# Performance work log

Measured on AMD Instinct MI355X. Metric: run time of the kernel, lower is better.

## Reference

```python
import jax, jax.numpy as jnp
import numpy as np

N0, N1, N2, N3 = 100000, 25000, 6250, 1600
DEG = 16
D_IN, D_H = 512, 256


def setup_inputs() -> dict:
    key = jax.random.key(0)
    ks = jax.random.split(key, 20)
    inp = {}
    inp["x"] = jax.random.normal(ks[0], (N0, D_IN), dtype=jnp.float32)
    # bipartite blocks: (src_ids into previous frontier, dst_ids into next frontier)
    inp["src0"] = jax.random.randint(ks[1], (N1 * DEG,), 0, N0)
    inp["dst0"] = jax.random.randint(ks[2], (N1 * DEG,), 0, N1)
    inp["src1"] = jax.random.randint(ks[3], (N2 * DEG,), 0, N1)
    inp["dst1"] = jax.random.randint(ks[4], (N2 * DEG,), 0, N2)
    inp["src2"] = jax.random.randint(ks[5], (N3 * DEG,), 0, N2)
    inp["dst2"] = jax.random.randint(ks[6], (N3 * DEG,), 0, N3)
    def xavier(k, shp):
        fan_in, fan_out = shp
        lim = jnp.sqrt(6.0 / (fan_in + fan_out))
        return jax.random.uniform(k, shp, jnp.float32, -lim, lim)
    inp["Ws0"] = xavier(ks[7], (D_IN, D_H)); inp["Wn0"] = xavier(ks[8], (D_IN, D_H)); inp["b0"] = jnp.zeros((D_H,), jnp.float32)
    inp["Ws1"] = xavier(ks[9], (D_H, D_H)); inp["Wn1"] = xavier(ks[10], (D_H, D_H)); inp["b1"] = jnp.zeros((D_H,), jnp.float32)
    inp["Ws2"] = xavier(ks[11], (D_H, D_H)); inp["Wn2"] = xavier(ks[12], (D_H, D_H)); inp["b2"] = jnp.zeros((D_H,), jnp.float32)
    inp["W_fc"] = xavier(ks[13], (D_H, D_H)); inp["b_fc"] = jnp.zeros((D_H,), jnp.float32)
    return inp


def _sage_mean(h, src, dst, n_dst, Ws, Wn, b):
    # DGL SAGEConv('mean') on a bipartite block: out = h_dst@Ws + mean_neigh@Wn + b
    h_dst = h[:n_dst]                                   # [n_dst, d]
    msg = h[src]                                        # [E, d] gather
    agg = jax.ops.segment_sum(msg, dst, num_segments=n_dst)
    deg = jax.ops.segment_sum(jnp.ones(src.shape, h.dtype), dst, num_segments=n_dst)
    mean = agg / jnp.maximum(deg, 1.0)[:, None]
    return h_dst @ Ws + mean @ Wn + b


def reference(x, src0, dst0, src1, dst1, src2, dst2,
              Ws0, Wn0, b0, Ws1, Wn1, b1, Ws2, Wn2, b2, W_fc, b_fc):
    h = _sage_mean(x, src0, dst0, N1, Ws0, Wn0, b0)
    h = jax.nn.relu(h)  # dropout is identity in eval mode
    h = _sage_mean(h, src1, dst1, N2, Ws1, Wn1, b1)
    h = jax.nn.relu(h)
    h = _sage_mean(h, src2, dst2, N3, Ws2, Wn2, b2)
    return h @ W_fc + b_fc
```

## Files before the change

### kernel.cpp

```cpp
#include <hip/hip_runtime.h>
#include <hip/hip_bf16.h>
#include <cstddef>
#include <cstdint>

#define N0 100000
#define N1 25000
#define N2 6250
#define N3 1600
#define DEG 16
#define D_IN 512
#define D_H 256

#define E0 (N1*DEG)
#define E1 (N2*DEG)
#define E2 (N3*DEG)

typedef _Float16 half_t;
typedef __attribute__((ext_vector_type(8))) _Float16 f16x8;
typedef __attribute__((ext_vector_type(4))) float f32x4;

#define XB 25000
#define WB 2304
#define HB (((E0+E1+E2) + 255) / 256)

__device__ __forceinline__ void gl_lds16(const void* g, void* l)
{
    __builtin_amdgcn_global_load_lds(
        (const __attribute__((address_space(1))) void*)g,
        (__attribute__((address_space(3))) void*)l,
        16, 0, 0);
}

__global__ __launch_bounds__(256)
void mega_conv_kernel(const float* __restrict__ x, half_t* __restrict__ xh,
                      const float* s0, const float* s1, const float* s2, const float* s3,
                      const float* s4, const float* s5, const float* s6,
                      half_t* t0, half_t* t1, half_t* t2, half_t* t3,
                      half_t* t4, half_t* t5, half_t* t6,
                      const int* __restrict__ d0, const int* __restrict__ d1,
                      const int* __restrict__ d2,
                      int* __restrict__ c0, int* __restrict__ c1, int* __restrict__ c2)
{
    const int bid = blockIdx.x;
    if (bid < XB) {
        const int id = bid * 256 + threadIdx.x;
        const float4* p = reinterpret_cast<const float4*>(x) + (size_t)id * 2;
        const float4 a = p[0], b = p[1];
        f16x8 o;
        o[0] = (half_t)a.x; o[1] = (half_t)a.y; o[2] = (half_t)a.z; o[3] = (half_t)a.w;
        o[4] = (half_t)b.x; o[5] = (half_t)b.y; o[6] = (half_t)b.z; o[7] = (half_t)b.w;
        *(reinterpret_cast<f16x8*>(xh) + id) = o;
    } else if (bid < XB + WB) {
        const int id = (bid - XB) * 256 + threadIdx.x;
        const float* src; half_t* dst; int kb; int e;
        if (id < 131072)      { src = s0; dst = t0; kb = 9; e = id; }
        else if (id < 262144) { src = s1; dst = t1; kb = 9; e = id - 131072; }
        else if (id < 327680) { src = s2; dst = t2; kb = 8; e = id - 262144; }
        else if (id < 393216) { src = s3; dst = t3; kb = 8; e = id - 327680; }
        else if (id < 458752) { src = s4; dst = t4; kb = 8; e = id - 393216; }
        else if (id < 524288) { src = s5; dst = t5; kb = 8; e = id - 458752; }
        else if (id < 589824) { src = s6; dst = t6; kb = 8; e = id - 524288; }
        else return;
        const int K = 1 << kb;
        const int nn = e >> kb, k = e & (K - 1);
        dst[((size_t)nn << kb) + k] = (half_t)src[(size_t)k * 256 + nn];
    } else {
        const int i = (bid - XB - WB) * 256 + threadIdx.x;
        if (i < E0)                atomicAdd(&c0[d0[i]], 1);
        else if (i < E0 + E1)      atomicAdd(&c1[d1[i - E0]], 1);
        else if (i < E0 + E1 + E2) atomicAdd(&c2[d2[i - E0 - E1]], 1);
    }
}

__global__ void fill3_kernel(const int* __restrict__ s0, const int* __restrict__ d0,
                             const int* __restrict__ s1, const int* __restrict__ d1,
                             const int* __restrict__ s2, const int* __restrict__ d2,
                             int* __restrict__ u0, int* __restrict__ u1, int* __restrict__ u2,
                             int* __restrict__ e0, int* __restrict__ e1, int* __restrict__ e2)
{
    const int i = blockIdx.x * 256 + threadIdx.x;
    if (i < E0) {
        const int p = atomicAdd(&u0[d0[i]], 1); e0[p] = s0[i];
    } else if (i < E0 + E1) {
        const int j = i - E0;
        const int p = atomicAdd(&u1[d1[j]], 1); e1[p] = s1[j];
    } else if (i < E0 + E1 + E2) {
        const int j = i - E0 - E1;
        const int p = atomicAdd(&u2[d2[j]], 1); e2[p] = s2[j];
    }
}

__global__ __launch_bounds__(1024)
void scan3_kernel(const int* __restrict__ c0, int* __restrict__ p0, int* __restrict__ u0,
                  const int* __restrict__ c1, int* __restrict__ p1, int* __restrict__ u1,
                  const int* __restrict__ c2, int* __restrict__ p2, int* __restrict__ u2)
{
    const int b = blockIdx.x;
    const int* cnt = (b == 0) ? c0 : (b == 1) ? c1 : c2;
    int* ptr = (b == 0) ? p0 : (b == 1) ? p1 : p2;
    int* cur = (b == 0) ? u0 : (b == 1) ? u1 : u2;
    const int n = (b == 0) ? N1 : (b == 1) ? N2 : N3;

    const int t = threadIdx.x;
    const int chunk = (n + 1023) >> 10;
    const int beg = t * chunk;
    const int end = min(n, beg + chunk);

    int sum = 0;
    for (int i = beg; i < end; ++i) sum += cnt[i];

    const int lane = t & 63, wid = t >> 6;
    int inc = sum;
    #pragma unroll
    for (int d = 1; d < 64; d <<= 1) {
        int u = __shfl_up(inc, d, 64);
        if (lane >= d) inc += u;
    }
    __shared__ int wtot[16];
    __shared__ int total_s;
    if (lane == 63) wtot[wid] = inc;
    __syncthreads();
    if (wid == 0) {
        int w = (lane < 16) ? wtot[lane] : 0;
        int ws = w;
        #pragma unroll
        for (int d = 1; d < 16; d <<= 1) {
            int u = __shfl_up(ws, d, 64);
            if (lane >= d) ws += u;
        }
        if (lane < 16) wtot[lane] = ws - w;
        if (lane == 15) total_s = ws;
    }
    __syncthreads();
    int run = (inc - sum) + wtot[wid];
    for (int i = beg; i < end; ++i) {
        ptr[i] = run; cur[i] = run;
        run += cnt[i];
    }
    if (t == 0) ptr[n] = total_s;
}

template<int K>
__global__ __launch_bounds__(256)
void csr_mean_f16(const half_t* __restrict__ h, const int* __restrict__ esrc,
                  const int* __restrict__ ptr, half_t* __restrict__ mean, int n)
{
    constexpr int TPN = K / 8;
    constexpr int NPB = 256 / TPN;
    const int node = blockIdx.x * NPB + threadIdx.x / TPN;
    const int lane = threadIdx.x % TPN;
    if (node >= n) return;
    const int beg = ptr[node], end = ptr[node + 1];
    float acc[8] = {};
    for (int base = beg; base < end; base += TPN) {
        const int rem = end - base;
        const int cnt = (rem < TPN) ? rem : TPN;
        const int myidx = (lane < cnt) ? esrc[base + lane] : 0;
        int j = 0;
        for (; j + 7 < cnt; j += 8) {
            int a[8];
            #pragma unroll
            for (int u = 0; u < 8; ++u) a[u] = __shfl(myidx, j + u, TPN);
            f16x8 v[8];
            #pragma unroll
            for (int u = 0; u < 8; ++u)
                v[u] = *reinterpret_cast<const f16x8*>(h + (size_t)a[u] * K + (size_t)lane * 8);
            #pragma unroll
            for (int u = 0; u < 8; ++u)
                #pragma unroll
                for (int i = 0; i < 8; ++i) acc[i] += (float)v[u][i];
        }
        for (; j < cnt; ++j) {
            const int a0 = __shfl(myidx, j, TPN);
            const f16x8 v0 = *reinterpret_cast<const f16x8*>(h + (size_t)a0 * K + (size_t)lane * 8);
            #pragma unroll
            for (int i = 0; i < 8; ++i) acc[i] += (float)v0[i];
        }
    }
    const float r = 1.0f / fmaxf((float)(end - beg), 1.0f);
    f16x8 o;
    #pragma unroll
    for (int i = 0; i < 8; ++i) o[i] = (half_t)(acc[i] * r);
    *reinterpret_cast<f16x8*>(mean + (size_t)node * K + (size_t)lane * 8) = o;
}

#define GBM 128
#define GBK 64

template<bool HAS_MEAN, bool RELU, bool OUT_F16>
__global__ __launch_bounds__(512)
void mfma_gemm(const half_t* __restrict__ A,
               const half_t* __restrict__ Mn,
               const half_t* __restrict__ WsT,
               const half_t* __restrict__ WnT,
               const float* __restrict__ bias,
               void* __restrict__ Cout,
               int M, int K)
{
    __shared__ half_t sA[GBM * GBK];
    __shared__ half_t sB[256 * GBK];

    const int tid  = threadIdx.x;
    const int wid  = tid >> 6;
    const int lane = tid & 63;
    const int wm   = wid >> 1;
    const int wn   = wid & 1;
    const int bm   = blockIdx.x * GBM;

    const int lrow = lane & 15;
    const int kg16 = (lane >> 4) << 4;

    f32x4 acc[2][8] = {};

    const int npass = HAS_MEAN ? 2 : 1;
    for (int pass = 0; pass < npass; ++pass) {
        const half_t* __restrict__ Ap = pass ? Mn : A;
        const half_t* __restrict__ Wp = pass ? WnT : WsT;

        for (int k0 = 0; k0 < K; k0 += GBK) {
            #pragma unroll
            for (int i = 0; i < 2; ++i) {
                const int Lb = ((i << 3) + wid) << 10;
                const int L  = Lb + (lane << 4);
                const int row = L >> 7;
                const int c   = (L & 127) ^ ((row & 7) << 4);
                gl_lds16(Ap + (size_t)(bm + row) * K + k0 + (c >> 1), sA + (Lb >> 1));
            }
            #pragma unroll
            for (int i = 0; i < 4; ++i) {
                const int Lb = ((i << 3) + wid) << 10;
                const int L  = Lb + (lane << 4);
                const int row = L >> 7;
                const int c   = (L & 127) ^ ((row & 7) << 4);
                gl_lds16(Wp + (size_t)row * K + k0 + (c >> 1), sB + (Lb >> 1));
            }
            __syncthreads();

            #pragma unroll
            for (int kk = 0; kk < 2; ++kk) {
                const int cb = (kk << 6) + kg16;
                f16x8 af[2];
                #pragma unroll
                for (int m = 0; m < 2; ++m) {
                    const int row = wm * 32 + m * 16 + lrow;
                    const int c = cb ^ ((row & 7) << 4);
                    af[m] = *reinterpret_cast<const f16x8*>(&sA[row * GBK + (c >> 1)]);
                }
                #pragma unroll
                for (int n = 0; n < 8; ++n) {
                    const int row = wn * 128 + n * 16 + lrow;
                    const int c = cb ^ ((row & 7) << 4);
                    const f16x8 bf = *reinterpret_cast<const f16x8*>(&sB[row * GBK + (c >> 1)]);
                    acc[0][n] = __builtin_amdgcn_mfma_f32_16x16x32_f16(af[0], bf, acc[0][n], 0, 0, 0);
                    acc[1][n] = __builtin_amdgcn_mfma_f32_16x16x32_f16(af[1], bf, acc[1][n], 0, 0, 0);
                }
            }
            __syncthreads();
        }
    }

    const int rgrp = lane >> 4;
    #pragma unroll
    for (int n = 0; n < 8; ++n) {
        const int col = wn * 128 + n * 16 + lrow;
        const float bv = bias[col];
        #pragma unroll
        for (int m = 0; m < 2; ++m) {
            #pragma unroll
            for (int r = 0; r < 4; ++r) {
                const int row = bm + wm * 32 + m * 16 + rgrp * 4 + r;
                if (row >= M) continue;
                float v = acc[m][n][r] + bv;
                if (RELU) v = fmaxf(v, 0.0f);
                if (OUT_F16) ((half_t*)Cout)[(size_t)row * 256 + col] = (half_t)v;
                else         ((float*)Cout)[(size_t)row * 256 + col] = v;
            }
        }
    }
}

static constexpr size_t align256(size_t x) { return (x + 255) & ~(size_t)255; }

extern "C" void kernel_launch(void* const* d_in, const int* in_sizes, int n_in,
                              void* d_out, int out_size, void* d_ws, size_t ws_size,
                              hipStream_t stream)
{
    const float* x    = (const float*)d_in[0];
    const int*  src0  = (const int*)d_in[1];
    const int*  dst0  = (const int*)d_in[2];
    const int*  src1  = (const int*)d_in[3];
    const int*  dst1  = (const int*)d_in[4];
    const int*  src2  = (const int*)d_in[5];
    const int*  dst2  = (const int*)d_in[6];
    const float* Ws0  = (const float*)d_in[7];
    const float* Wn0  = (const float*)d_in[8];
    const float* b0   = (const float*)d_in[9];
    const float* Ws1  = (const float*)d_in[10];
    const float* Wn1  = (const float*)d_in[11];
    const float* b1   = (const float*)d_in[12];
    const float* Ws2  = (const float*)d_in[13];
    const float* Wn2  = (const float*)d_in[14];
    const float* b2   = (const float*)d_in[15];
    const float* W_fc = (const float*)d_in[16];
    const float* b_fc = (const float*)d_in[17];
    float* out = (float*)d_out;

    char* ws = (char*)d_ws;
    size_t off = 0;
    const size_t cntA_off = off; off = align256(off + (size_t)(N1 + N2 + N3) * 4);
    const size_t ptr0_off = off; off = align256(off + (size_t)(N1 + 1) * 4);
    const size_t ptr1_off = off; off = align256(off + (size_t)(N2 + 1) * 4);
    const size_t ptr2_off = off; off = align256(off + (size_t)(N3 + 1) * 4);
    const size_t cur0_off = off; off = align256(off + (size_t)N1 * 4);
    const size_t cur1_off = off; off = align256(off + (size_t)N2 * 4);
    const size_t cur2_off = off; off = align256(off + (size_t)N3 * 4);
    const size_t es0_off  = off; off = align256(off + (size_t)E0 * 4);
    const size_t es1_off  = off; off = align256(off + (size_t)E1 * 4);
    const size_t es2_off  = off; off = align256(off + (size_t)E2 * 4);
    const size_t xh_off   = off; off = align256(off + (size_t)N0 * D_IN * 2);
    const size_t mean_off = off; off = align256(off + (size_t)N1 * D_IN * 2);
    const size_t h0_off   = off; off = align256(off + (size_t)N1 * D_H * 2);
    const size_t h1_off   = off; off = align256(off + (size_t)N2 * D_H * 2);
    const size_t h2_off   = off; off = align256(off + (size_t)N3 * D_H * 2);
    const size_t wt0_off  = off; off = align256(off + (size_t)D_IN * D_H * 2);
    const size_t wt1_off  = off; off = align256(off + (size_t)D_IN * D_H * 2);
    const size_t wt2_off  = off; off = align256(off + (size_t)D_H * D_H * 2);
    const size_t wt3_off  = off; off = align256(off + (size_t)D_H * D_H * 2);
    const size_t wt4_off  = off; off = align256(off + (size_t)D_H * D_H * 2);
    const size_t wt5_off  = off; off = align256(off + (size_t)D_H * D_H * 2);
    const size_t wt6_off  = off; off = align256(off + (size_t)D_H * D_H * 2);

    int* cnt0 = (int*)(ws + cntA_off);
    int* cnt1 = cnt0 + N1;
    int* cnt2 = cnt1 + N2;
    int* ptr0 = (int*)(ws + ptr0_off);
    int* ptr1 = (int*)(ws + ptr1_off);
    int* ptr2 = (int*)(ws + ptr2_off);
    int* cur0 = (int*)(ws + cur0_off);
    int* cur1 = (int*)(ws + cur1_off);
    int* cur2 = (int*)(ws + cur2_off);
    int* es0  = (int*)(ws + es0_off);
    int* es1  = (int*)(ws + es1_off);
    int* es2  = (int*)(ws + es2_off);
    half_t* xh   = (half_t*)(ws + xh_off);
    half_t* mean = (half_t*)(ws + mean_off);
    half_t* h0   = (half_t*)(ws + h0_off);
    half_t* h1   = (half_t*)(ws + h1_off);
    half_t* h2   = (half_t*)(ws + h2_off);
    half_t* WsT0 = (half_t*)(ws + wt0_off);
    half_t* WnT0 = (half_t*)(ws + wt1_off);
    half_t* WsT1 = (half_t*)(ws + wt2_off);
    half_t* WnT1 = (half_t*)(ws + wt3_off);
    half_t* WsT2 = (half_t*)(ws + wt4_off);
    half_t* WnT2 = (half_t*)(ws + wt5_off);
    half_t* WfcT = (half_t*)(ws + wt6_off);

    hipMemsetAsync(cnt0, 0, (size_t)(N1 + N2 + N3) * 4, stream);
    mega_conv_kernel<<<XB + WB + HB, 256, 0, stream>>>(
        x, xh,
        Ws0, Wn0, Ws1, Wn1, Ws2, Wn2, W_fc,
        WsT0, WnT0, WsT1, WnT1, WsT2, WnT2, WfcT,
        dst0, dst1, dst2, cnt0, cnt1, cnt2);
    scan3_kernel<<<3, 1024, 0, stream>>>(cnt0, ptr0, cur0, cnt1, ptr1, cur1, cnt2, ptr2, cur2);
    {
        const int tot = E0 + E1 + E2;
        fill3_kernel<<<(tot + 255) / 256, 256, 0, stream>>>(
            src0, dst0, src1, dst1, src2, dst2, cur0, cur1, cur2, es0, es1, es2);
    }

    {
        constexpr int NPB = 256 / (D_IN / 8);
        csr_mean_f16<D_IN><<<(N1 + NPB - 1) / NPB, 256, 0, stream>>>(xh, es0, ptr0, mean, N1);
        mfma_gemm<true, true, true><<<(N1 + GBM - 1) / GBM, 512, 0, stream>>>(
            xh, mean, WsT0, WnT0, b0, h0, N1, D_IN);
    }
    {
        constexpr int NPB = 256 / (D_H / 8);
        csr_mean_f16<D_H><<<(N2 + NPB - 1) / NPB, 256, 0, stream>>>(h0, es1, ptr1, mean, N2);
        mfma_gemm<true, true, true><<<(N2 + GBM - 1) / GBM, 512, 0, stream>>>(
            h0, mean, WsT1, WnT1, b1, h1, N2, D_H);
    }
    {
        constexpr int NPB = 256 / (D_H / 8);
        csr_mean_f16<D_H><<<(N3 + NPB - 1) / NPB, 256, 0, stream>>>(h1, es2, ptr2, mean, N3);
        mfma_gemm<true, false, true><<<(N3 + GBM - 1) / GBM, 512, 0, stream>>>(
            h1, mean, WsT2, WnT2, b2, h2, N3, D_H);
    }
    mfma_gemm<false, false, false><<<(N3 + GBM - 1) / GBM, 512, 0, stream>>>(
        h2, nullptr, WfcT, nullptr, b_fc, out, N3, D_H);
}
```

Baseline: 319.8 us.

## Fuse neighbor mean aggregation into the SAGE GEMM kernel via shared memory

```diff
diff --git a/kernel.cpp b/kernel.cpp
--- a/kernel.cpp
+++ b/kernel.cpp
@@ -22,14 +22,6 @@
 #define XB 25000
 #define WB 2304
 #define HB (((E0+E1+E2) + 255) / 256)
-
-__device__ __forceinline__ void gl_lds16(const void* g, void* l)
-{
-    __builtin_amdgcn_global_load_lds(
-        (const __attribute__((address_space(1))) void*)g,
-        (__attribute__((address_space(3))) void*)l,
-        16, 0, 0);
-}
 
 __global__ __launch_bounds__(256)
 void mega_conv_kernel(const float* __restrict__ x, half_t* __restrict__ xh,
@@ -140,135 +132,139 @@
     if (t == 0) ptr[n] = total_s;
 }
 
-template<int K>
+#define BM 32
+#define LB 40
+
+template<int K, bool MEAN, bool RELU, bool OUT_F16>
 __global__ __launch_bounds__(256)
-void csr_mean_f16(const half_t* __restrict__ h, const int* __restrict__ esrc,
-                  const int* __restrict__ ptr, half_t* __restrict__ mean, int n)
-{
-    constexpr int TPN = K / 8;
-    constexpr int NPB = 256 / TPN;
-    const int node = blockIdx.x * NPB + threadIdx.x / TPN;
-    const int lane = threadIdx.x % TPN;
-    if (node >= n) return;
-    const int beg = ptr[node], end = ptr[node + 1];
-    float acc[8] = {};
-    for (int base = beg; base < end; base += TPN) {
-        const int rem = end - base;
-        const int cnt = (rem < TPN) ? rem : TPN;
-        const int myidx = (lane < cnt) ? esrc[base + lane] : 0;
-        int j = 0;
-        for (; j + 7 < cnt; j += 8) {
-            int a[8];
-            #pragma unroll
-            for (int u = 0; u < 8; ++u) a[u] = __shfl(myidx, j + u, TPN);
-            f16x8 v[8];
-            #pragma unroll
-            for (int u = 0; u < 8; ++u)
-                v[u] = *reinterpret_cast<const f16x8*>(h + (size_t)a[u] * K + (size_t)lane * 8);
-            #pragma unroll
-            for (int u = 0; u < 8; ++u)
-                #pragma unroll
-                for (int i = 0; i < 8; ++i) acc[i] += (float)v[u][i];
-        }
-        for (; j < cnt; ++j) {
-            const int a0 = __shfl(myidx, j, TPN);
-            const f16x8 v0 = *reinterpret_cast<const f16x8*>(h + (size_t)a0 * K + (size_t)lane * 8);
-            #pragma unroll
-            for (int i = 0; i < 8; ++i) acc[i] += (float)v0[i];
-        }
-    }
-    const float r = 1.0f / fmaxf((float)(end - beg), 1.0f);
-    f16x8 o;
-    #pragma unroll
-    for (int i = 0; i < 8; ++i) o[i] = (half_t)(acc[i] * r);
-    *reinterpret_cast<f16x8*>(mean + (size_t)node * K + (size_t)lane * 8) = o;
-}
-
-#define GBM 128
-#define GBK 64
-
-template<bool HAS_MEAN, bool RELU, bool OUT_F16>
-__global__ __launch_bounds__(512)
-void mfma_gemm(const half_t* __restrict__ A,
-               const half_t* __restrict__ Mn,
-               const half_t* __restrict__ WsT,
-               const half_t* __restrict__ WnT,
-               const float* __restrict__ bias,
-               void* __restrict__ Cout,
-               int M, int K)
-{
-    __shared__ half_t sA[GBM * GBK];
-    __shared__ half_t sB[256 * GBK];
+void fused_sage(const half_t* __restrict__ feat,
+                const int* __restrict__ esrc,
+                const int* __restrict__ ptr,
+                const half_t* __restrict__ WsT,
+                const half_t* __restrict__ WnT,
+                const float* __restrict__ bias,
+                void* __restrict__ Cout,
+                int M)
+{
+    constexpr int LM = K + 8;
+    __shared__ half_t sA[BM * LB];
+    __shared__ half_t sBs[256 * LB];
+    __shared__ half_t sBn[MEAN ? 256 * LB : 1];
+    __shared__ half_t meanS[MEAN ? BM * LM : 1];
 
     const int tid  = threadIdx.x;
+    const int bm   = blockIdx.x * BM;
     const int wid  = tid >> 6;
     const int lane = tid & 63;
-    const int wm   = wid >> 1;
-    const int wn   = wid & 1;
-    const int bm   = blockIdx.x * GBM;
-
     const int lrow = lane & 15;
-    const int kg16 = (lane >> 4) << 4;
-
-    f32x4 acc[2][8] = {};
-
-    const int npass = HAS_MEAN ? 2 : 1;
-    for (int pass = 0; pass < npass; ++pass) {
-        const half_t* __restrict__ Ap = pass ? Mn : A;
-        const half_t* __restrict__ Wp = pass ? WnT : WsT;
-
-        for (int k0 = 0; k0 < K; k0 += GBK) {
-            #pragma unroll
-            for (int i = 0; i < 2; ++i) {
-                const int Lb = ((i << 3) + wid) << 10;
-                const int L  = Lb + (lane << 4);
-                const int row = L >> 7;
-                const int c   = (L & 127) ^ ((row & 7) << 4);
-                gl_lds16(Ap + (size_t)(bm + row) * K + k0 + (c >> 1), sA + (Lb >> 1));
-            }
-            #pragma unroll
-            for (int i = 0; i < 4; ++i) {
-                const int Lb = ((i << 3) + wid) << 10;
-                const int L  = Lb + (lane << 4);
-                const int row = L >> 7;
-                const int c   = (L & 127) ^ ((row & 7) << 4);
-                gl_lds16(Wp + (size_t)row * K + k0 + (c >> 1), sB + (Lb >> 1));
-            }
-            __syncthreads();
-
-            #pragma unroll
-            for (int kk = 0; kk < 2; ++kk) {
-                const int cb = (kk << 6) + kg16;
-                f16x8 af[2];
-                #pragma unroll
-                for (int m = 0; m < 2; ++m) {
-                    const int row = wm * 32 + m * 16 + lrow;
-                    const int c = cb ^ ((row & 7) << 4);
-                    af[m] = *reinterpret_cast<const f16x8*>(&sA[row * GBK + (c >> 1)]);
-                }
-                #pragma unroll
-                for (int n = 0; n < 8; ++n) {
-                    const int row = wn * 128 + n * 16 + lrow;
-                    const int c = cb ^ ((row & 7) << 4);
-                    const f16x8 bf = *reinterpret_cast<const f16x8*>(&sB[row * GBK + (c >> 1)]);
-                    acc[0][n] = __builtin_amdgcn_mfma_f32_16x16x32_f16(af[0], bf, acc[0][n], 0, 0, 0);
-                    acc[1][n] = __builtin_amdgcn_mfma_f32_16x16x32_f16(af[1], bf, acc[1][n], 0, 0, 0);
+    const int kgrp = lane >> 4;
+
+    if (MEAN) {
+        constexpr int TPN = K / 8;
+        constexpr int NG  = 256 / TPN;
+        const int grp = tid / TPN;
+        const int gl  = tid % TPN;
+        #pragma unroll
+        for (int it = 0; it < BM / NG; ++it) {
+            const int loc = it * NG + grp;
+            const int r   = bm + loc;
+            float acc[8] = {};
+            int deg = 0;
+            if (r < M) {
+                const int beg = ptr[r], end = ptr[r + 1];
+                deg = end - beg;
+                for (int base = beg; base < end; base += TPN) {
+                    const int rem = end - base;
+                    const int cnt = (rem < TPN) ? rem : TPN;
+                    const int myidx = (gl < cnt) ? esrc[base + gl] : 0;
+                    int j = 0;
+                    for (; j + 7 < cnt; j += 8) {
+                        int a[8];
+                        #pragma unroll
+                        for (int u = 0; u < 8; ++u) a[u] = __shfl(myidx, j + u, TPN);
+                        f16x8 v[8];
+                        #pragma unroll
+                        for (int u = 0; u < 8; ++u)
+                            v[u] = *reinterpret_cast<const f16x8*>(feat + (size_t)a[u] * K + (size_t)gl * 8);
+                        #pragma unroll
+                        for (int u = 0; u < 8; ++u)
+                            #pragma unroll
+                            for (int i = 0; i < 8; ++i) acc[i] += (float)v[u][i];
+                    }
+                    for (; j < cnt; ++j) {
+                        const int a0 = __shfl(myidx, j, TPN);
+                        const f16x8 v0 = *reinterpret_cast<const f16x8*>(feat + (size_t)a0 * K + (size_t)gl * 8);
+                        #pragma unroll
+                        for (int i = 0; i < 8; ++i) acc[i] += (float)v0[i];
+                    }
                 }
             }
-            __syncthreads();
-        }
+            const float rcp = 1.0f / fmaxf((float)deg, 1.0f);
+            f16x8 o;
+            #pragma unroll
+            for (int i = 0; i < 8; ++i) o[i] = (half_t)(acc[i] * rcp);
+            *reinterpret_cast<f16x8*>(&meanS[loc * LM + gl * 8]) = o;
+        }
+    }
+    __syncthreads();
+
+    f32x4 acc[2][4] = {};
+
+    for (int k0 = 0; k0 < K; k0 += 32) {
+        if (tid < 128) {
+            const int row = tid >> 2;
+            const int kq  = (tid & 3) * 8;
+            f16x8 v = {};
+            if (bm + row < M)
+                v = *reinterpret_cast<const f16x8*>(feat + (size_t)(bm + row) * K + k0 + kq);
+            *reinterpret_cast<f16x8*>(&sA[row * LB + kq]) = v;
+        }
+        {
+            const int kq = (tid & 3) * 8;
+            #pragma unroll
+            for (int j = 0; j < 4; ++j) {
+                const int row = (tid >> 2) + 64 * j;
+                *reinterpret_cast<f16x8*>(&sBs[row * LB + kq]) =
+                    *reinterpret_cast<const f16x8*>(WsT + (size_t)row * K + k0 + kq);
+                if (MEAN)
+                    *reinterpret_cast<f16x8*>(&sBn[row * LB + kq]) =
+                        *reinterpret_cast<const f16x8*>(WnT + (size_t)row * K + k0 + kq);
+            }
+        }
+        __syncthreads();
+
+        f16x8 af0[2], af1[2];
+        #pragma unroll
+        for (int m = 0; m < 2; ++m) {
+            af0[m] = *reinterpret_cast<const f16x8*>(&sA[(m * 16 + lrow) * LB + kgrp * 8]);
+            if (MEAN)
+                af1[m] = *reinterpret_cast<const f16x8*>(&meanS[(m * 16 + lrow) * LM + k0 + kgrp * 8]);
+        }
+        #pragma unroll
+        for (int n = 0; n < 4; ++n) {
+            const int brow = (wid * 64 + n * 16 + lrow) * LB + kgrp * 8;
+            const f16x8 bfs = *reinterpret_cast<const f16x8*>(&sBs[brow]);
+            acc[0][n] = __builtin_amdgcn_mfma_f32_16x16x32_f16(af0[0], bfs, acc[0][n], 0, 0, 0);
+            acc[1][n] = __builtin_amdgcn_mfma_f32_16x16x32_f16(af0[1], bfs, acc[1][n], 0, 0, 0);
+            if (MEAN) {
+                const f16x8 bfn = *reinterpret_cast<const f16x8*>(&sBn[brow]);
+                acc[0][n] = __builtin_amdgcn_mfma_f32_16x16x32_f16(af1[0], bfn, acc[0][n], 0, 0, 0);
+                acc[1][n] = __builtin_amdgcn_mfma_f32_16x16x32_f16(af1[1], bfn, acc[1][n], 0, 0, 0);
+            }
+        }
+        __syncthreads();
     }
 
     const int rgrp = lane >> 4;
     #pragma unroll
-    for (int n = 0; n < 8; ++n) {
-        const int col = wn * 128 + n * 16 + lrow;
+    for (int n = 0; n < 4; ++n) {
+        const int col = wid * 64 + n * 16 + lrow;
         const float bv = bias[col];
         #pragma unroll
         for (int m = 0; m < 2; ++m) {
             #pragma unroll
             for (int r = 0; r < 4; ++r) {
-                const int row = bm + wm * 32 + m * 16 + rgrp * 4 + r;
+                const int row = bm + m * 16 + rgrp * 4 + r;
                 if (row >= M) continue;
                 float v = acc[m][n][r] + bv;
                 if (RELU) v = fmaxf(v, 0.0f);
@@ -318,7 +314,6 @@
     const size_t es1_off  = off; off = align256(off + (size_t)E1 * 4);
     const size_t es2_off  = off; off = align256(off + (size_t)E2 * 4);
     const size_t xh_off   = off; off = align256(off + (size_t)N0 * D_IN * 2);
-    const size_t mean_off = off; off = align256(off + (size_t)N1 * D_IN * 2);
     const size_t h0_off   = off; off = align256(off + (size_t)N1 * D_H * 2);
     const size_t h1_off   = off; off = align256(off + (size_t)N2 * D_H * 2);
     const size_t h2_off   = off; off = align256(off + (size_t)N3 * D_H * 2);
@@ -343,7 +338,6 @@
     int* es1  = (int*)(ws + es1_off);
     int* es2  = (int*)(ws + es2_off);
     half_t* xh   = (half_t*)(ws + xh_off);
-    half_t* mean = (half_t*)(ws + mean_off);
     half_t* h0   = (half_t*)(ws + h0_off);
     half_t* h1   = (half_t*)(ws + h1_off);
     half_t* h2   = (half_t*)(ws + h2_off);
@@ -368,24 +362,12 @@
             src0, dst0, src1, dst1, src2, dst2, cur0, cur1, cur2, es0, es1, es2);
     }
 
-    {
-        constexpr int NPB = 256 / (D_IN / 8);
-        csr_mean_f16<D_IN><<<(N1 + NPB - 1) / NPB, 256, 0, stream>>>(xh, es0, ptr0, mean, N1);
-        mfma_gemm<true, true, true><<<(N1 + GBM - 1) / GBM, 512, 0, stream>>>(
-            xh, mean, WsT0, WnT0, b0, h0, N1, D_IN);
-    }
-    {
-        constexpr int NPB = 256 / (D_H / 8);
-        csr_mean_f16<D_H><<<(N2 + NPB - 1) / NPB, 256, 0, stream>>>(h0, es1, ptr1, mean, N2);
-        mfma_gemm<true, true, true><<<(N2 + GBM - 1) / GBM, 512, 0, stream>>>(
-            h0, mean, WsT1, WnT1, b1, h1, N2, D_H);
-    }
-    {
-        constexpr int NPB = 256 / (D_H / 8);
-        csr_mean_f16<D_H><<<(N3 + NPB - 1) / NPB, 256, 0, stream>>>(h1, es2, ptr2, mean, N3);
-        mfma_gemm<true, false, true><<<(N3 + GBM - 1) / GBM, 512, 0, stream>>>(
-            h1, mean, WsT2, WnT2, b2, h2, N3, D_H);
-    }
-    mfma_gemm<false, false, false><<<(N3 + GBM - 1) / GBM, 512, 0, stream>>>(
-        h2, nullptr, WfcT, nullptr, b_fc, out, N3, D_H);
-}
+    fused_sage<D_IN, true, true, true><<<(N1 + BM - 1) / BM, 256, 0, stream>>>(
+        xh, es0, ptr0, WsT0, WnT0, b0, h0, N1);
+    fused_sage<D_H, true, true, true><<<(N2 + BM - 1) / BM, 256, 0, stream>>>(
+        h0, es1, ptr1, WsT1, WnT1, b1, h1, N2);
+    fused_sage<D_H, true, false, true><<<(N3 + BM - 1) / BM, 256, 0, stream>>>(
+        h1, es2, ptr2, WsT2, WnT2, b2, h2, N3);
+    fused_sage<D_H, false, false, false><<<(N3 + BM - 1) / BM, 256, 0, stream>>>(
+        h2, nullptr, nullptr, WfcT, nullptr, b_fc, out, N3);
+}
```

New measurement: 333.0 us. 1.04x slower.
